# Kernel optimization log

Measured on AMD Instinct MI355X. Metric: run time of the kernel, lower is better.

Reference implementation:

```python
import math
import itertools
import jax, jax.numpy as jnp
import numpy as np

QUALITY = 95
FACTOR = (200.0 - 2.0 * QUALITY) / 100.0  # quality>=50 branch -> 0.1

# ---- constant tables (match original torch Parameters) ----
_Y = np.array([
    [16, 11, 10, 16, 24, 40, 51, 61],
    [12, 12, 14, 19, 26, 58, 60, 55],
    [14, 13, 16, 24, 40, 57, 69, 56],
    [14, 17, 22, 29, 51, 87, 80, 62],
    [18, 22, 37, 56, 68, 109, 103, 77],
    [24, 35, 55, 64, 81, 104, 113, 92],
    [49, 64, 78, 87, 103, 121, 120, 101],
    [72, 92, 95, 98, 112, 100, 103, 99]], dtype=np.float32)
Y_TABLE = jnp.asarray(_Y.T)
_C = np.full((8, 8), 99.0, dtype=np.float32)
_C[:4, :4] = np.array([[17, 18, 24, 47], [18, 21, 26, 66],
                       [24, 26, 56, 99], [47, 66, 99, 99]], dtype=np.float32).T
C_TABLE = jnp.asarray(_C)

RGB2YCBCR = jnp.asarray(np.array([
    [0.299, 0.587, 0.114],
    [-0.168736, -0.331264, 0.5],
    [0.5, -0.418688, -0.081312]], dtype=np.float32))
YCBCR2RGB = jnp.asarray(np.array([
    [1.0, 0.0, 1.402],
    [1.0, -0.344136, -0.714136],
    [1.0, 1.772, 0.0]], dtype=np.float32))

_cosmat = np.cos((2 * np.arange(8)[:, None] + 1) * np.arange(8)[None, :] * np.pi / 16).astype(np.float32)  # [x,u]
DCT_T = jnp.asarray(np.einsum('xu,yv->xyuv', _cosmat, _cosmat))   # tensor[x,y,u,v]
IDCT_T = jnp.asarray(np.einsum('ux,vy->xyuv', _cosmat, _cosmat))  # cos((2u+1)x..)cos((2v+1)y..)
_alpha = np.array([1.0 / np.sqrt(2)] + [1.0] * 7, dtype=np.float32)
ALPHA = jnp.asarray(np.outer(_alpha, _alpha))
DCT_SCALE = ALPHA * 0.25


def diff_round(x):
    s = jnp.zeros_like(x)
    for n in range(1, 10):
        s = s + ((-1.0) ** (n + 1) / n) * jnp.sin(2.0 * math.pi * n * x)
    return x - s / math.pi


def _avgpool2(x):  # [B,H,W] -> [B,H/2,W/2]
    b, h, w = x.shape
    return x.reshape(b, h // 2, 2, w // 2, 2).mean(axis=(2, 4))


def _block_split(x):  # [B,H,W] -> [B,N,8,8]
    b, h, w = x.shape
    return x.reshape(b, h // 8, 8, w // 8, 8).transpose(0, 1, 3, 2, 4).reshape(b, -1, 8, 8)


def _block_merge(p, h, w):  # [B,N,8,8] -> [B,h,w]
    b = p.shape[0]
    return p.reshape(b, h // 8, w // 8, 8, 8).transpose(0, 1, 3, 2, 4).reshape(b, h, w)


def _compress_component(comp, table):
    blocks = _block_split(comp) - 128.0
    dct = DCT_SCALE * jnp.einsum('bnxy,xyuv->bnuv', blocks, DCT_T)
    return diff_round(dct / (table * FACTOR))


def _decompress_component(q, table, h, w):
    d = q * (table * FACTOR)
    idct = 0.25 * jnp.einsum('bnxy,xyuv->bnuv', d * ALPHA, IDCT_T) + 128.0
    return _block_merge(idct, h, w)


def _diffjpeg(x):
    b, c, h, w = x.shape
    img = x * 255.0
    # RGB -> YCbCr (pixel @ RGB2YCBCR.T) + shift
    ycbcr = jnp.einsum('bchw,oc->bhwo', img, RGB2YCBCR) + jnp.array([0.0, 128.0, 128.0], dtype=x.dtype)
    y = ycbcr[..., 0]
    cb = _avgpool2(ycbcr[..., 1])
    cr = _avgpool2(ycbcr[..., 2])
    # compress
    yq = _compress_component(y, Y_TABLE)
    cbq = _compress_component(cb, C_TABLE)
    crq = _compress_component(cr, C_TABLE)
    # decompress
    y2 = _decompress_component(yq, Y_TABLE, h, w)
    cb2 = _decompress_component(cbq, C_TABLE, h // 2, w // 2)
    cr2 = _decompress_component(crq, C_TABLE, h // 2, w // 2)
    cb_up = jnp.repeat(jnp.repeat(cb2, 2, axis=1), 2, axis=2)
    cr_up = jnp.repeat(jnp.repeat(cr2, 2, axis=1), 2, axis=2)
    ycc = jnp.stack([y2, cb_up, cr_up], axis=3)  # [B,H,W,3]
    rgb = jnp.einsum('bhwc,oc->bhwo', ycc + jnp.array([0.0, -128.0, -128.0], dtype=x.dtype), YCBCR2RGB)
    rgb = rgb.transpose(0, 3, 1, 2)  # [B,3,H,W]
    rgb = jnp.clip(rgb, 0.0, 255.0)
    return rgb / 255.0


def setup_inputs() -> dict:
    key = jax.random.key(0)
    x = jax.random.uniform(key, (16, 3, 512, 512), dtype=jnp.float32)
    return {"x": x}


def reference(x):
    return _diffjpeg(x)
```

## Files before the change

kernel.cpp:

```cpp
#include <hip/hip_runtime.h>


__device__ constexpr float YTAB8[8][8] = {
    {16, 12, 14, 14, 18, 24, 49, 72},
    {11, 12, 13, 17, 22, 35, 64, 92},
    {10, 14, 16, 22, 37, 55, 78, 95},
    {16, 19, 24, 29, 56, 64, 87, 98},
    {24, 26, 40, 51, 68, 81, 103, 112},
    {40, 58, 57, 87, 109, 104, 121, 100},
    {51, 60, 69, 80, 103, 113, 120, 103},
    {61, 55, 56, 62, 77, 92, 101, 99}};

__device__ constexpr float CTAB8[8][8] = {
    {17, 18, 24, 47, 99, 99, 99, 99},
    {18, 21, 26, 66, 99, 99, 99, 99},
    {24, 26, 56, 99, 99, 99, 99, 99},
    {47, 66, 99, 99, 99, 99, 99, 99},
    {99, 99, 99, 99, 99, 99, 99, 99},
    {99, 99, 99, 99, 99, 99, 99, 99},
    {99, 99, 99, 99, 99, 99, 99, 99},
    {99, 99, 99, 99, 99, 99, 99, 99}};

#define C1f 0.9807852804032304f
#define C2f 0.9238795325112867f
#define C3f 0.8314696123025452f
#define C4f 0.7071067811865476f
#define C5f 0.5555702330196022f
#define C6f 0.3826834323650898f
#define C7f 0.1950903220161283f

__device__ __forceinline__ void dct8(float y[8]) {
    float e0=y[0]+y[7], e1=y[1]+y[6], e2=y[2]+y[5], e3=y[3]+y[4];
    float o0=y[0]-y[7], o1=y[1]-y[6], o2=y[2]-y[5], o3=y[3]-y[4];
    float t0=e0+e3, t1=e1+e2, d0=e0-e3, d1=e1-e2;
    y[0]=t0+t1; y[4]=(t0-t1)*C4f;
    y[2]=d0*C2f+d1*C6f; y[6]=d0*C6f-d1*C2f;
    y[1]=o0*C1f+o1*C3f+o2*C5f+o3*C7f;
    y[3]=o0*C3f-o1*C7f-o2*C1f-o3*C5f;
    y[5]=o0*C5f-o1*C1f+o2*C7f+o3*C3f;
    y[7]=o0*C7f-o1*C5f+o2*C3f-o3*C1f;
}

__device__ __forceinline__ void idct8(float y[8]) {
    float a=y[4]*C4f, p=y[0]+a, m=y[0]-a;
    float q=y[2]*C2f+y[6]*C6f, w=y[2]*C6f-y[6]*C2f;
    float E0=p+q, E1=m+w, E2=m-w, E3=p-q;
    float O0=y[1]*C1f+y[3]*C3f+y[5]*C5f+y[7]*C7f;
    float O1=y[1]*C3f-y[3]*C7f-y[5]*C1f-y[7]*C5f;
    float O2=y[1]*C5f-y[3]*C1f+y[5]*C7f+y[7]*C3f;
    float O3=y[1]*C7f-y[3]*C5f+y[5]*C3f-y[7]*C1f;
    y[0]=E0+O0; y[7]=E0-O0; y[1]=E1+O1; y[6]=E1-O1;
    y[2]=E2+O2; y[5]=E2-O2; y[3]=E3+O3; y[4]=E3-O3;
}

__device__ __forceinline__ void transpose8(float y[8]) {
    const int lane = threadIdx.x & 63;
#pragma unroll
    for (int s = 1; s <= 4; s <<= 1) {
        const bool upper = (lane & (s << 3)) != 0;
#pragma unroll
        for (int j = 0; j < 8; ++j) {
            if ((j & s) == 0) {
                float a = y[j], b2 = y[j | s];
                float t = upper ? a : b2;
                t = __shfl_xor(t, s << 3, 64);
                if (upper) y[j] = t; else y[j | s] = t;
            }
        }
    }
}

__device__ __forceinline__ float diff_round_f(float x) {
    float f = __builtin_amdgcn_fractf(x);
    float sc = __builtin_amdgcn_sinf(f);
    float c1v = __builtin_amdgcn_cosf(f);
    float twoc = 2.0f * c1v;
    float sp = 0.0f, acc = 0.0f;
    const float coef[9] = {1.0f, -0.5f, 1.0f/3.0f, -0.25f, 0.2f,
                           -1.0f/6.0f, 1.0f/7.0f, -0.125f, 1.0f/9.0f};
#pragma unroll
    for (int n = 0; n < 9; ++n) {
        acc += coef[n] * sc;
        float sn = twoc * sc - sp;
        sp = sc; sc = sn;
    }
    return x - acc * 0.3183098861837907f;
}

__device__ __forceinline__ void jpeg_block(float y[8], const float* qs, int r) {
    dct8(y); transpose8(y); dct8(y);
#pragma unroll
    for (int j = 0; j < 8; ++j) {
        float s1v = qs[2 * (j * 8 + r)];
        float s2v = qs[2 * (j * 8 + r) + 1];
        y[j] = diff_round_f(y[j] * s1v) * s2v;
    }
    idct8(y); transpose8(y); idct8(y);
}

__global__ __launch_bounds__(64, 4) void diffjpeg_kernel(
        const float* __restrict__ x, float* __restrict__ out) {
    __shared__ float QS[2][128];
    __shared__ float PL[2][8][17];
    __shared__ float CL[2][8][17];

    const int tid = threadIdx.x;
    const int r = tid >> 3;
    const int b = tid & 7;

    {
        const int u = r, v = b;
        float ty = YTAB8[u][v] * 0.1f;
        float tc = CTAB8[u][v] * 0.1f;
        float aa = 0.25f * ((u == 0) ? C4f : 1.0f) * ((v == 0) ? C4f : 1.0f);
        QS[0][2 * tid] = aa / ty; QS[0][2 * tid + 1] = aa * ty;
        QS[1][2 * tid] = aa / tc; QS[1][2 * tid + 1] = aa * tc;
    }

    const int img = blockIdx.y;
    const int sy = (blockIdx.x >> 4) * 16;
    const int sx = (blockIdx.x & 15) * 32;
    const size_t plane = (size_t)512 * 512;
    const float* src = x + (size_t)img * 3 * plane;
    float* dst = out + (size_t)img * 3 * plane;

    const int br = b >> 2, bc = b & 3;
    const int py = sy + br * 8 + r;
    const int px = sx + bc * 8;

    float y[8];
    {
        const float* p = src + (size_t)py * 512 + px;
        float4 R0 = *(const float4*)(p);
        float4 R1 = *(const float4*)(p + 4);
        float4 G0 = *(const float4*)(p + plane);
        float4 G1 = *(const float4*)(p + plane + 4);
        float4 B0 = *(const float4*)(p + 2 * plane);
        float4 B1 = *(const float4*)(p + 2 * plane + 4);
        y[0] = 76.245f*R0.x + 149.685f*G0.x + 29.07f*B0.x - 128.0f;
        y[1] = 76.245f*R0.y + 149.685f*G0.y + 29.07f*B0.y - 128.0f;
        y[2] = 76.245f*R0.z + 149.685f*G0.z + 29.07f*B0.z - 128.0f;
        y[3] = 76.245f*R0.w + 149.685f*G0.w + 29.07f*B0.w - 128.0f;
        y[4] = 76.245f*R1.x + 149.685f*G1.x + 29.07f*B1.x - 128.0f;
        y[5] = 76.245f*R1.y + 149.685f*G1.y + 29.07f*B1.y - 128.0f;
        y[6] = 76.245f*R1.z + 149.685f*G1.z + 29.07f*B1.z - 128.0f;
        y[7] = 76.245f*R1.w + 149.685f*G1.w + 29.07f*B1.w - 128.0f;
        float rh0=R0.x+R0.y, rh1=R0.z+R0.w, rh2=R1.x+R1.y, rh3=R1.z+R1.w;
        float gh0=G0.x+G0.y, gh1=G0.z+G0.w, gh2=G1.x+G1.y, gh3=G1.z+G1.w;
        float bh0=B0.x+B0.y, bh1=B0.z+B0.w, bh2=B1.x+B1.y, bh3=B1.z+B1.w;
        const float kbr = -10.75692f, kbg = -21.11808f, kbb = 31.875f;
        const float krr =  31.875f,   krg = -26.69136f, krb = -5.18364f;
        float cb[4], cr[4];
        cb[0]=kbr*rh0+kbg*gh0+kbb*bh0; cb[1]=kbr*rh1+kbg*gh1+kbb*bh1;
        cb[2]=kbr*rh2+kbg*gh2+kbb*bh2; cb[3]=kbr*rh3+kbg*gh3+kbb*bh3;
        cr[0]=krr*rh0+krg*gh0+krb*bh0; cr[1]=krr*rh1+krg*gh1+krb*bh1;
        cr[2]=krr*rh2+krg*gh2+krb*bh2; cr[3]=krr*rh3+krg*gh3+krb*bh3;
#pragma unroll
        for (int k = 0; k < 4; ++k) {
            cb[k] += __shfl_xor(cb[k], 8, 64);
            cr[k] += __shfl_xor(cr[k], 8, 64);
        }
        if (!(r & 1)) {
            const int prow = br * 4 + (r >> 1);
            const int pc = bc * 4;
#pragma unroll
            for (int k = 0; k < 4; ++k) {
                PL[0][prow][pc + k] = cb[k];
                PL[1][prow][pc + k] = cr[k];
            }
        }
    }
    __syncthreads();

    jpeg_block(y, QS[0], r);

    {
        const int ch = (b >> 1) & 1;
        const int cblk = b & 1;
        float c[8];
#pragma unroll
        for (int j = 0; j < 8; ++j) c[j] = PL[ch][r][cblk * 8 + j];
        jpeg_block(c, QS[1], r);
        if (b < 4) {
#pragma unroll
            for (int j = 0; j < 8; ++j) CL[ch][r][cblk * 8 + j] = c[j];
        }
    }
    __syncthreads();

    {
        const int prow = br * 4 + (r >> 1);
        const int pc = bc * 4;
        float cbv[4], crv[4];
#pragma unroll
        for (int jj = 0; jj < 4; ++jj) {
            cbv[jj] = CL[0][prow][pc + jj];
            crv[jj] = CL[1][prow][pc + jj];
        }
        float oR[8], oG[8], oB[8];
#pragma unroll
        for (int j = 0; j < 8; ++j) {
            float cb = cbv[j >> 1], cr = crv[j >> 1];
            float yv = y[j] + 128.0f;
            float R = yv + 1.402f * cr;
            float G = yv - 0.344136f * cb - 0.714136f * cr;
            float B = yv + 1.772f * cb;
            oR[j] = fminf(fmaxf(R, 0.0f), 255.0f) * (1.0f / 255.0f);
            oG[j] = fminf(fmaxf(G, 0.0f), 255.0f) * (1.0f / 255.0f);
            oB[j] = fminf(fmaxf(B, 0.0f), 255.0f) * (1.0f / 255.0f);
        }
        float* p = dst + (size_t)py * 512 + px;
        *(float4*)(p)                 = make_float4(oR[0], oR[1], oR[2], oR[3]);
        *(float4*)(p + 4)             = make_float4(oR[4], oR[5], oR[6], oR[7]);
        *(float4*)(p + plane)         = make_float4(oG[0], oG[1], oG[2], oG[3]);
        *(float4*)(p + plane + 4)     = make_float4(oG[4], oG[5], oG[6], oG[7]);
        *(float4*)(p + 2 * plane)     = make_float4(oB[0], oB[1], oB[2], oB[3]);
        *(float4*)(p + 2 * plane + 4) = make_float4(oB[4], oB[5], oB[6], oB[7]);
    }
}

extern "C" void kernel_launch(void* const* d_in, const int* in_sizes, int n_in,
                              void* d_out, int out_size, void* d_ws, size_t ws_size,
                              hipStream_t stream) {
    const float* x = (const float*)d_in[0];
    float* out = (float*)d_out;
    dim3 grid(512, 16);
    dim3 block(64);
    diffjpeg_kernel<<<grid, block, 0, stream>>>(x, out);
}
```

Before: 24.88 us.

## Pack two waves per block and replace block barriers with wave-local LDS fences

Each block now holds two independent 64-lane waves, each processing its own 16x32 strip with private LDS staging. The mid-kernel __syncthreads calls become wave-level fences that wait on LDS counters, with a single block barrier left after the shared quant-table setup. The setup work is split so each wave fills one table, and the color-conversion epilogue stores one channel at a time to cut live registers. This aims to lower per-block launch and barrier overhead and raise occupancy, but the correctness of the wave-local fence depends on wave-synchronous LDS behavior.

```diff
diff --git a/kernel.cpp b/kernel.cpp
--- a/kernel.cpp
+++ b/kernel.cpp
@@ -70,6 +70,12 @@
     }
 }
 
+__device__ __forceinline__ void wave_lds_fence() {
+    __builtin_amdgcn_wave_barrier();
+    asm volatile("s_waitcnt lgkmcnt(0)" ::: "memory");
+    __builtin_amdgcn_wave_barrier();
+}
+
 __device__ __forceinline__ float diff_round_f(float x) {
     float f = __builtin_amdgcn_fractf(x);
     float sc = __builtin_amdgcn_sinf(f);
@@ -98,28 +104,33 @@
     idct8(y); transpose8(y); idct8(y);
 }
 
-__global__ __launch_bounds__(64, 4) void diffjpeg_kernel(
+__global__ __launch_bounds__(128, 6) void diffjpeg_kernel(
         const float* __restrict__ x, float* __restrict__ out) {
     __shared__ float QS[2][128];
-    __shared__ float PL[2][8][17];
-    __shared__ float CL[2][8][17];
+    __shared__ float PL[2][2][8][17];
+    __shared__ float CL[2][2][8][17];
 
     const int tid = threadIdx.x;
-    const int r = tid >> 3;
-    const int b = tid & 7;
-
-    {
-        const int u = r, v = b;
-        float ty = YTAB8[u][v] * 0.1f;
-        float tc = CTAB8[u][v] * 0.1f;
+
+    {
+        int type = tid >> 6;
+        int k = tid & 63, u = k >> 3, v = k & 7;
+        float t = (type ? CTAB8[u][v] : YTAB8[u][v]) * 0.1f;
         float aa = 0.25f * ((u == 0) ? C4f : 1.0f) * ((v == 0) ? C4f : 1.0f);
-        QS[0][2 * tid] = aa / ty; QS[0][2 * tid + 1] = aa * ty;
-        QS[1][2 * tid] = aa / tc; QS[1][2 * tid + 1] = aa * tc;
-    }
+        QS[type][2 * k]     = aa / t;
+        QS[type][2 * k + 1] = aa * t;
+    }
+    __syncthreads();
+
+    const int wv = tid >> 6;
+    const int lane = tid & 63;
+    const int r = lane >> 3;
+    const int b = lane & 7;
 
     const int img = blockIdx.y;
-    const int sy = (blockIdx.x >> 4) * 16;
-    const int sx = (blockIdx.x & 15) * 32;
+    const int strip = blockIdx.x * 2 + wv;
+    const int sy = (strip >> 4) * 16;
+    const int sx = (strip & 15) * 32;
     const size_t plane = (size_t)512 * 512;
     const float* src = x + (size_t)img * 3 * plane;
     float* dst = out + (size_t)img * 3 * plane;
@@ -165,12 +176,12 @@
             const int pc = bc * 4;
 #pragma unroll
             for (int k = 0; k < 4; ++k) {
-                PL[0][prow][pc + k] = cb[k];
-                PL[1][prow][pc + k] = cr[k];
+                PL[wv][0][prow][pc + k] = cb[k];
+                PL[wv][1][prow][pc + k] = cr[k];
             }
         }
     }
-    __syncthreads();
+    wave_lds_fence();
 
     jpeg_block(y, QS[0], r);
 
@@ -179,14 +190,14 @@
         const int cblk = b & 1;
         float c[8];
 #pragma unroll
-        for (int j = 0; j < 8; ++j) c[j] = PL[ch][r][cblk * 8 + j];
+        for (int j = 0; j < 8; ++j) c[j] = PL[wv][ch][r][cblk * 8 + j];
         jpeg_block(c, QS[1], r);
         if (b < 4) {
 #pragma unroll
-            for (int j = 0; j < 8; ++j) CL[ch][r][cblk * 8 + j] = c[j];
-        }
-    }
-    __syncthreads();
+            for (int j = 0; j < 8; ++j) CL[wv][ch][r][cblk * 8 + j] = c[j];
+        }
+    }
+    wave_lds_fence();
 
     {
         const int prow = br * 4 + (r >> 1);
@@ -194,28 +205,32 @@
         float cbv[4], crv[4];
 #pragma unroll
         for (int jj = 0; jj < 4; ++jj) {
-            cbv[jj] = CL[0][prow][pc + jj];
-            crv[jj] = CL[1][prow][pc + jj];
-        }
-        float oR[8], oG[8], oB[8];
-#pragma unroll
-        for (int j = 0; j < 8; ++j) {
-            float cb = cbv[j >> 1], cr = crv[j >> 1];
-            float yv = y[j] + 128.0f;
-            float R = yv + 1.402f * cr;
-            float G = yv - 0.344136f * cb - 0.714136f * cr;
-            float B = yv + 1.772f * cb;
-            oR[j] = fminf(fmaxf(R, 0.0f), 255.0f) * (1.0f / 255.0f);
-            oG[j] = fminf(fmaxf(G, 0.0f), 255.0f) * (1.0f / 255.0f);
-            oB[j] = fminf(fmaxf(B, 0.0f), 255.0f) * (1.0f / 255.0f);
+            cbv[jj] = CL[wv][0][prow][pc + jj];
+            crv[jj] = CL[wv][1][prow][pc + jj];
         }
         float* p = dst + (size_t)py * 512 + px;
-        *(float4*)(p)                 = make_float4(oR[0], oR[1], oR[2], oR[3]);
-        *(float4*)(p + 4)             = make_float4(oR[4], oR[5], oR[6], oR[7]);
-        *(float4*)(p + plane)         = make_float4(oG[0], oG[1], oG[2], oG[3]);
-        *(float4*)(p + plane + 4)     = make_float4(oG[4], oG[5], oG[6], oG[7]);
-        *(float4*)(p + 2 * plane)     = make_float4(oB[0], oB[1], oB[2], oB[3]);
-        *(float4*)(p + 2 * plane + 4) = make_float4(oB[4], oB[5], oB[6], oB[7]);
+        float o[8];
+#pragma unroll
+        for (int j = 0; j < 8; ++j) {
+            float v = (y[j] + 128.0f) + 1.402f * crv[j >> 1];
+            o[j] = fminf(fmaxf(v, 0.0f), 255.0f) * (1.0f / 255.0f);
+        }
+        *(float4*)(p)     = make_float4(o[0], o[1], o[2], o[3]);
+        *(float4*)(p + 4) = make_float4(o[4], o[5], o[6], o[7]);
+#pragma unroll
+        for (int j = 0; j < 8; ++j) {
+            float v = (y[j] + 128.0f) - 0.344136f * cbv[j >> 1] - 0.714136f * crv[j >> 1];
+            o[j] = fminf(fmaxf(v, 0.0f), 255.0f) * (1.0f / 255.0f);
+        }
+        *(float4*)(p + plane)     = make_float4(o[0], o[1], o[2], o[3]);
+        *(float4*)(p + plane + 4) = make_float4(o[4], o[5], o[6], o[7]);
+#pragma unroll
+        for (int j = 0; j < 8; ++j) {
+            float v = (y[j] + 128.0f) + 1.772f * cbv[j >> 1];
+            o[j] = fminf(fmaxf(v, 0.0f), 255.0f) * (1.0f / 255.0f);
+        }
+        *(float4*)(p + 2 * plane)     = make_float4(o[0], o[1], o[2], o[3]);
+        *(float4*)(p + 2 * plane + 4) = make_float4(o[4], o[5], o[6], o[7]);
     }
 }
 
@@ -224,7 +239,7 @@
                               hipStream_t stream) {
     const float* x = (const float*)d_in[0];
     float* out = (float*)d_out;
-    dim3 grid(512, 16);
-    dim3 block(64);
+    dim3 grid(256, 16);
+    dim3 block(128);
     diffjpeg_kernel<<<grid, block, 0, stream>>>(x, out);
 }
```

Result: faster. 24.23 us (-2.6%).
